# Kernel tuning notes

Measured on AMD Instinct MI355X. Metric: run time of the kernel, lower is better.

Reference implementation:

```python
import jax, jax.numpy as jnp
import numpy as np

N, E, IN_C, DIM, OUT_C, G = 40000, 640000, 128, 128, 16, 256
BN_EPS = 1e-5

def setup_inputs() -> dict:
    key = jax.random.key(0)
    ks = jax.random.split(key, 24)
    x = jax.random.normal(ks[0], (N, IN_C), dtype=jnp.float32)
    edge_index = jax.random.randint(ks[1], (2, E), 0, N, dtype=jnp.int32)
    batch = jnp.sort(jax.random.randint(ks[2], (N,), 0, G, dtype=jnp.int32))
    s = 1.0 / np.sqrt(DIM)
    # layer 1 (in_channels -> dim)
    W1_0 = jax.random.uniform(ks[3], (IN_C, DIM), jnp.float32, -s, s)
    b1_0 = jnp.zeros((DIM,), jnp.float32)
    g_0 = jnp.ones((DIM,), jnp.float32)
    bt_0 = jnp.zeros((DIM,), jnp.float32)
    W2_0 = jax.random.uniform(ks[4], (DIM, DIM), jnp.float32, -s, s)
    b2_0 = jnp.zeros((DIM,), jnp.float32)
    # layers 2-5 stacked (dim -> dim)
    W1s = jax.random.uniform(ks[5], (4, DIM, DIM), jnp.float32, -s, s)
    b1s = jnp.zeros((4, DIM), jnp.float32)
    gs = jnp.ones((4, DIM), jnp.float32)
    bts = jnp.zeros((4, DIM), jnp.float32)
    W2s = jax.random.uniform(ks[6], (4, DIM, DIM), jnp.float32, -s, s)
    b2s = jnp.zeros((4, DIM), jnp.float32)
    lin1_W = jax.random.uniform(ks[7], (DIM, DIM), jnp.float32, -s, s)
    lin1_b = jnp.zeros((DIM,), jnp.float32)
    lin2_W = jax.random.uniform(ks[8], (DIM, OUT_C), jnp.float32, -s, s)
    lin2_b = jnp.zeros((OUT_C,), jnp.float32)
    return dict(x=x, edge_index=edge_index, batch=batch, num_graphs=G,
                W1_0=W1_0, b1_0=b1_0, g_0=g_0, bt_0=bt_0, W2_0=W2_0, b2_0=b2_0,
                W1s=W1s, b1s=b1s, gs=gs, bts=bts, W2s=W2s, b2s=b2s,
                lin1_W=lin1_W, lin1_b=lin1_b, lin2_W=lin2_W, lin2_b=lin2_b)

def _gin_layer(x, src, dst, W1, b1, g, bt, W2, b2):
    # GIN aggregation: (1 + eps) * x_i + sum_{j in N(i)} x_j, eps = 0
    agg = jax.ops.segment_sum(x[src], dst, num_segments=x.shape[0])
    h = (x + agg) @ W1 + b1
    # BatchNorm1d over nodes (training-mode batch stats, biased variance)
    mu = h.mean(axis=0)
    var = h.var(axis=0)
    h = (h - mu) * jax.lax.rsqrt(var + BN_EPS) * g + bt
    h = jax.nn.relu(h)
    return jax.nn.relu(h @ W2 + b2)

def reference(x, edge_index, batch, num_graphs,
              W1_0, b1_0, g_0, bt_0, W2_0, b2_0,
              W1s, b1s, gs, bts, W2s, b2s,
              lin1_W, lin1_b, lin2_W, lin2_b):
    src, dst = edge_index[0], edge_index[1]
    h = _gin_layer(x, src, dst, W1_0, b1_0, g_0, bt_0, W2_0, b2_0)
    for i in range(4):
        h = _gin_layer(h, src, dst, W1s[i], b1s[i], gs[i], bts[i], W2s[i], b2s[i])
    x1 = h  # dropout p=0.2 in eval mode = identity
    pooled = jax.ops.segment_sum(x1, batch, num_segments=num_graphs)  # [G, DIM]
    out = jax.nn.relu(pooled @ lin1_W + lin1_b)
    out = out @ lin2_W + lin2_b
    return (jax.nn.log_softmax(out, axis=-1), x1)
```

## Files before the change

### kernel.cpp

```cpp
#include <hip/hip_runtime.h>

namespace {

constexpr int N    = 40000;
constexpr int E    = 640000;
constexpr int DIM  = 128;
constexpr int NG   = 256;
constexpr int OUTC = 16;
constexpr float BN_EPS = 1e-5f;

typedef __attribute__((ext_vector_type(8))) short bf16x8;
typedef __attribute__((ext_vector_type(4))) float f32x4;
typedef __attribute__((ext_vector_type(2))) float f32x2;

__device__ __forceinline__ void atomAddF(float* p, float v) {
  unsafeAtomicAdd(p, v);
}

__device__ __forceinline__ unsigned b16r(float f) {
  unsigned u = __float_as_uint(f);
  return (u + 0x7fffu + ((u >> 16) & 1u)) >> 16;
}
__device__ __forceinline__ unsigned pack2(float a, float b) {
  return b16r(a) | (b16r(b) << 16);
}

__device__ __forceinline__ unsigned pk4_fp8(float4 v) {
  unsigned u = __builtin_amdgcn_cvt_pk_fp8_f32(v.x, v.y, 0, false);
  u = __builtin_amdgcn_cvt_pk_fp8_f32(v.z, v.w, u, true);
  return u;
}
__device__ __forceinline__ void addfp8x4(float* a, unsigned u) {
  f32x2 lo = __builtin_amdgcn_cvt_pk_f32_fp8(u, false);
  f32x2 hi = __builtin_amdgcn_cvt_pk_f32_fp8(u, true);
  a[0] += lo[0]; a[1] += lo[1]; a[2] += hi[0]; a[3] += hi[1];
}
__device__ __forceinline__ void add16(float* a, const uint4 v) {
  addfp8x4(a, v.x); addfp8x4(a + 4, v.y); addfp8x4(a + 8, v.z); addfp8x4(a + 12, v.w);
}

__device__ __forceinline__ bf16x8 bnrelu8(bf16x8 a, const float* sc, const float* sh) {
  union { bf16x8 v; unsigned u[4]; } in, out;
  in.v = a;
#pragma unroll
  for (int p = 0; p < 4; ++p) {
    float lo = __uint_as_float(in.u[p] << 16);
    float hi = __uint_as_float(in.u[p] & 0xffff0000u);
    lo = fmaxf(fmaf(lo, sc[2 * p], sh[2 * p]), 0.f);
    hi = fmaxf(fmaf(hi, sc[2 * p + 1], sh[2 * p + 1]), 0.f);
    out.u[p] = pack2(lo, hi);
  }
  return out.v;
}

constexpr int CVT_B   = (N * DIM / 4) / 256;
constexpr int HIST_B  = E / 256;
constexpr int TRANS_B = 10 * DIM / 4;

__global__ __launch_bounds__(256) void prep_kernel(const float* __restrict__ x,
                                                   unsigned char* __restrict__ xf8,
                                                   const int* __restrict__ dst,
                                                   int* __restrict__ deg,
                                                   const float* __restrict__ W1_0,
                                                   const float* __restrict__ W2_0,
                                                   const float* __restrict__ W1s,
                                                   const float* __restrict__ W2s,
                                                   ushort* __restrict__ Wt) {
  const int b = blockIdx.x;
  if (b < CVT_B) {
    const int i = b * 256 + threadIdx.x;
    float4 v = ((const float4*)x)[i];
    ((unsigned*)xf8)[i] = pk4_fp8(v);
  } else if (b < CVT_B + HIST_B) {
    const int e = (b - CVT_B) * 256 + threadIdx.x;
    atomicAdd(&deg[dst[e]], 1);
  } else {
    const int ob   = (b - CVT_B - HIST_B) * 4 + (threadIdx.x >> 6);
    const int lane = threadIdx.x & 63;
    const int m = ob >> 7;
    const int c = ob & 127;
    const int l = m >> 1;
    const float* W;
    if (l == 0) W = (m & 1) ? W2_0 : W1_0;
    else        W = ((m & 1) ? W2s : W1s) + (size_t)(l - 1) * DIM * DIM;
    const int k = lane * 2;
    float f0 = W[(size_t)k * DIM + c];
    float f1 = W[(size_t)(k + 1) * DIM + c];
    ((unsigned*)Wt)[((size_t)m * DIM + c) * 64 + lane] = pack2(f0, f1);
  }
}


__global__ __launch_bounds__(256) void alloc_kernel(const int* __restrict__ deg,
                                                    int* __restrict__ counter,
                                                    int* __restrict__ start,
                                                    int* __restrict__ cursor) {
  const int i    = blockIdx.x * blockDim.x + threadIdx.x;
  const int lane = threadIdx.x & 63;
  int d = (i < N) ? deg[i] : 0;
  int incl = d;
#pragma unroll
  for (int o = 1; o < 64; o <<= 1) {
    int v = __shfl_up(incl, o, 64);
    if (lane >= o) incl += v;
  }
  int base = 0;
  if (lane == 63) base = atomicAdd(counter, incl);
  base = __shfl(base, 63, 64);
  int s0 = base + incl - d;
  if (i < N) { start[i] = s0; cursor[i] = s0; }
}

__global__ void fill_kernel(const int* __restrict__ src, const int* __restrict__ dst,
                            int* __restrict__ cursor, int* __restrict__ col) {
  int e = blockIdx.x * blockDim.x + threadIdx.x;
  if (e < E) {
    int p = atomicAdd(&cursor[dst[e]], 1);
    col[p] = src[e];
  }
}


__global__ __launch_bounds__(512) void gin1_fused(const unsigned char* __restrict__ xf8,
                                                  const int* __restrict__ start,
                                                  const int* __restrict__ deg,
                                                  const int* __restrict__ col,
                                                  const ushort* __restrict__ Wt1,
                                                  const float* __restrict__ b1,
                                                  ushort* __restrict__ h,
                                                  float* __restrict__ stats8) {
  __shared__ uint4 tile4[64 * 16];
  const int tid   = threadIdx.x;
  const int node0 = blockIdx.x * 64;

  {
    const int r = tid >> 3;
    const int l = tid & 7;
    const int node = node0 + r;
    const uint4* __restrict__ x16 = (const uint4*)xf8;
    float a[16];
#pragma unroll
    for (int i = 0; i < 16; ++i) a[i] = 0.f;
    add16(a, x16[(size_t)node * 8 + l]);
    const int b = start[node], n = deg[node];
    int k = 0;
    for (; k + 4 <= n; k += 4) {
      int j0 = col[b + k], j1 = col[b + k + 1], j2 = col[b + k + 2], j3 = col[b + k + 3];
      uint4 v0 = x16[(size_t)j0 * 8 + l];
      uint4 v1 = x16[(size_t)j1 * 8 + l];
      uint4 v2 = x16[(size_t)j2 * 8 + l];
      uint4 v3 = x16[(size_t)j3 * 8 + l];
      add16(a, v0); add16(a, v1); add16(a, v2); add16(a, v3);
    }
    for (; k < n; ++k) add16(a, x16[(size_t)col[b + k] * 8 + l]);
    uint4 o0 = {pack2(a[0], a[1]), pack2(a[2], a[3]), pack2(a[4], a[5]), pack2(a[6], a[7])};
    uint4 o1 = {pack2(a[8], a[9]), pack2(a[10], a[11]), pack2(a[12], a[13]), pack2(a[14], a[15])};
    const int sw = (r << 1) & 15;
    tile4[r * 16 + ((2 * l) ^ sw)]     = o0;
    tile4[r * 16 + ((2 * l + 1) ^ sw)] = o1;
  }
  __syncthreads();

  const int w    = tid >> 6;
  const int lane = tid & 63;
  const int rh   = __builtin_amdgcn_readfirstlane(w >> 2);
  const int c0   = __builtin_amdgcn_readfirstlane((w & 3) * 32);
  const int lr   = lane & 15;
  const int lg   = lane >> 4;

  const ushort* __restrict__ brow = Wt1 + (size_t)(c0 + lr) * DIM + lg * 8;
  const bf16x8* __restrict__ tb   = (const bf16x8*)tile4;

  f32x4 acc00 = {0, 0, 0, 0}, acc01 = {0, 0, 0, 0}, acc10 = {0, 0, 0, 0}, acc11 = {0, 0, 0, 0};
  const int r0 = rh * 32 + lr, r1 = rh * 32 + 16 + lr;
  const int sw0 = (r0 << 1) & 15, sw1 = (r1 << 1) & 15;
#pragma unroll
  for (int ks = 0; ks < 4; ++ks) {
    bf16x8 a0 = tb[r0 * 16 + ((lg + ks * 4) ^ sw0)];
    bf16x8 a1 = tb[r1 * 16 + ((lg + ks * 4) ^ sw1)];
    bf16x8 b0 = *(const bf16x8*)(brow + ks * 32);
    bf16x8 b1v = *(const bf16x8*)(brow + 16 * DIM + ks * 32);
    acc00 = __builtin_amdgcn_mfma_f32_16x16x32_bf16(a0, b0, acc00, 0, 0, 0);
    acc01 = __builtin_amdgcn_mfma_f32_16x16x32_bf16(a0, b1v, acc01, 0, 0, 0);
    acc10 = __builtin_amdgcn_mfma_f32_16x16x32_bf16(a1, b0, acc10, 0, 0, 0);
    acc11 = __builtin_amdgcn_mfma_f32_16x16x32_bf16(a1, b1v, acc11, 0, 0, 0);
  }

  const float bia0 = b1[c0 + lr];
  const float bia1 = b1[c0 + 16 + lr];
  float s[2] = {0, 0}, q[2] = {0, 0};
  f32x4 accs[2][2] = {{acc00, acc01}, {acc10, acc11}};
#pragma unroll
  for (int rf = 0; rf < 2; ++rf) {
#pragma unroll
    for (int cf = 0; cf < 2; ++cf) {
      const int colidx = c0 + cf * 16 + lr;
      const float bb = cf ? bia1 : bia0;
#pragma unroll
      for (int rg = 0; rg < 4; ++rg) {
        float v = accs[rf][cf][rg] + bb;
        const int row = node0 + rh * 32 + rf * 16 + lg * 4 + rg;
        h[(size_t)row * DIM + colidx] = (ushort)b16r(v);
        s[cf] += v; q[cf] = fmaf(v, v, q[cf]);
      }
    }
  }
#pragma unroll
  for (int cf = 0; cf < 2; ++cf) {
    float ss = s[cf], qq = q[cf];
    ss += __shfl_xor(ss, 16); ss += __shfl_xor(ss, 32);
    qq += __shfl_xor(qq, 16); qq += __shfl_xor(qq, 32);
    if (lg == 0) {
      float* st = stats8 + (blockIdx.x & 7) * 2 * DIM;
      atomAddF(&st[c0 + cf * 16 + lr], ss);
      atomAddF(&st[DIM + c0 + cf * 16 + lr], qq);
    }
  }
}


template <int F32OUT>
__global__ __launch_bounds__(256) void gin2_fused(const ushort* __restrict__ h,
                                                  const float* __restrict__ stats8,
                                                  const float* __restrict__ gamma,
                                                  const float* __restrict__ beta,
                                                  const ushort* __restrict__ Wt2,
                                                  const float* __restrict__ b2,
                                                  unsigned char* __restrict__ xf8,
                                                  float* __restrict__ outf) {
  __shared__ float lsc[DIM], lsh[DIM];
  const int tid = threadIdx.x;
  if (tid < DIM) {
    float s = 0.f, q = 0.f;
#pragma unroll
    for (int p = 0; p < 8; ++p) {
      s += stats8[p * 2 * DIM + tid];
      q += stats8[p * 2 * DIM + DIM + tid];
    }
    const float inv_n = 1.0f / N;
    float mu  = s * inv_n;
    float var = q * inv_n - mu * mu;
    float sc  = gamma[tid] * rsqrtf(var + BN_EPS);
    lsc[tid] = sc;
    lsh[tid] = beta[tid] - mu * sc;
  }
  __syncthreads();

  const int lane = tid & 63;
  const int c0   = __builtin_amdgcn_readfirstlane((tid >> 6) * 32);
  const int lr   = lane & 15;
  const int lg   = lane >> 4;
  const int row0 = blockIdx.x * 32;

  const ushort* __restrict__ arow = h + (size_t)(row0 + lr) * DIM + lg * 8;
  const ushort* __restrict__ brow = Wt2 + (size_t)(c0 + lr) * DIM + lg * 8;

  f32x4 acc00 = {0, 0, 0, 0}, acc01 = {0, 0, 0, 0}, acc10 = {0, 0, 0, 0}, acc11 = {0, 0, 0, 0};

#pragma unroll
  for (int ks = 0; ks < 4; ++ks) {
    const int ch0 = lg * 8 + ks * 32;
    float sc[8], sh[8];
    *(float4*)(sc)     = *(const float4*)&lsc[ch0];
    *(float4*)(sc + 4) = *(const float4*)&lsc[ch0 + 4];
    *(float4*)(sh)     = *(const float4*)&lsh[ch0];
    *(float4*)(sh + 4) = *(const float4*)&lsh[ch0 + 4];
    bf16x8 a0 = bnrelu8(*(const bf16x8*)(arow + ks * 32), sc, sh);
    bf16x8 a1 = bnrelu8(*(const bf16x8*)(arow + 16 * DIM + ks * 32), sc, sh);
    bf16x8 b0 = *(const bf16x8*)(brow + ks * 32);
    bf16x8 b1 = *(const bf16x8*)(brow + 16 * DIM + ks * 32);
    acc00 = __builtin_amdgcn_mfma_f32_16x16x32_bf16(a0, b0, acc00, 0, 0, 0);
    acc01 = __builtin_amdgcn_mfma_f32_16x16x32_bf16(a0, b1, acc01, 0, 0, 0);
    acc10 = __builtin_amdgcn_mfma_f32_16x16x32_bf16(a1, b0, acc10, 0, 0, 0);
    acc11 = __builtin_amdgcn_mfma_f32_16x16x32_bf16(a1, b1, acc11, 0, 0, 0);
  }

  const float bia0 = b2[c0 + lr];
  const float bia1 = b2[c0 + 16 + lr];
  f32x4 accs[2][2] = {{acc00, acc01}, {acc10, acc11}};
#pragma unroll
  for (int rf = 0; rf < 2; ++rf) {
#pragma unroll
    for (int cf = 0; cf < 2; ++cf) {
      const int colidx = c0 + cf * 16 + lr;
      const float bb = cf ? bia1 : bia0;
#pragma unroll
      for (int rg = 0; rg < 4; ++rg) {
        float v = fmaxf(accs[rf][cf][rg] + bb, 0.f);
        const int row = row0 + rf * 16 + lg * 4 + rg;
        if (F32OUT) {
          outf[(size_t)row * DIM + colidx] = v;
        } else {
          float vp = __shfl_xor(v, 1);
          if (!(lr & 1)) {
            unsigned pk = __builtin_amdgcn_cvt_pk_fp8_f32(v, vp, 0, false);
            *(ushort*)(xf8 + (size_t)row * DIM + colidx) = (ushort)pk;
          }
        }
      }
    }
  }
}


__global__ __launch_bounds__(256) void pool_kernel(const float* __restrict__ x1,
                                                   const int* __restrict__ batch,
                                                   float* __restrict__ pooled) {
  const int grp  = (blockIdx.x * blockDim.x + threadIdx.x) >> 5;
  const int lane = threadIdx.x & 31;
  const int node0 = grp * 64;
  if (node0 >= N) return;
  const int end = (node0 + 64 < N) ? (node0 + 64) : N;
  float4 acc = {0, 0, 0, 0};
  int cur = batch[node0];
  for (int n = node0; n < end; ++n) {
    int b = batch[n];
    if (b != cur) {
      atomAddF(&pooled[(size_t)cur * DIM + lane * 4 + 0], acc.x);
      atomAddF(&pooled[(size_t)cur * DIM + lane * 4 + 1], acc.y);
      atomAddF(&pooled[(size_t)cur * DIM + lane * 4 + 2], acc.z);
      atomAddF(&pooled[(size_t)cur * DIM + lane * 4 + 3], acc.w);
      acc = {0, 0, 0, 0};
      cur = b;
    }
    float4 v = ((const float4*)x1)[(size_t)n * 32 + lane];
    acc.x += v.x; acc.y += v.y; acc.z += v.z; acc.w += v.w;
  }
  atomAddF(&pooled[(size_t)cur * DIM + lane * 4 + 0], acc.x);
  atomAddF(&pooled[(size_t)cur * DIM + lane * 4 + 1], acc.y);
  atomAddF(&pooled[(size_t)cur * DIM + lane * 4 + 2], acc.z);
  atomAddF(&pooled[(size_t)cur * DIM + lane * 4 + 3], acc.w);
}


__global__ __launch_bounds__(128) void mlp_kernel(const float* __restrict__ pooled,
                                                  const float* __restrict__ W1,
                                                  const float* __restrict__ b1,
                                                  const float* __restrict__ W2,
                                                  const float* __restrict__ b2,
                                                  float* __restrict__ out) {
  const int gidx = blockIdx.x;
  const int t    = threadIdx.x;
  __shared__ float p[DIM], a1[DIM];
  p[t] = pooled[(size_t)gidx * DIM + t];
  __syncthreads();
  float acc = b1[t];
  for (int k = 0; k < DIM; ++k) acc = fmaf(p[k], W1[(size_t)k * DIM + t], acc);
  a1[t] = fmaxf(acc, 0.f);
  __syncthreads();
  if (t < OUTC) {
    float o = b2[t];
    for (int k = 0; k < DIM; ++k) o = fmaf(a1[k], W2[(size_t)k * OUTC + t], o);
    float m = o;
    for (int s = 8; s >= 1; s >>= 1) m = fmaxf(m, __shfl_xor(m, s, 16));
    float e = __expf(o - m);
    float se = e;
    for (int s = 8; s >= 1; s >>= 1) se += __shfl_xor(se, s, 16);
    out[(size_t)gidx * OUTC + t] = o - m - __logf(se);
  }
}

}

extern "C" void kernel_launch(void* const* d_in, const int* in_sizes, int n_in,
                              void* d_out, int out_size, void* d_ws, size_t ws_size,
                              hipStream_t stream) {
  const float* x     = (const float*)d_in[0];
  const int*   ei    = (const int*)d_in[1];
  const int*   batch = (const int*)d_in[2];
  const float* W1_0  = (const float*)d_in[4];
  const float* b1_0  = (const float*)d_in[5];
  const float* g_0   = (const float*)d_in[6];
  const float* bt_0  = (const float*)d_in[7];
  const float* W2_0  = (const float*)d_in[8];
  const float* b2_0  = (const float*)d_in[9];
  const float* W1s   = (const float*)d_in[10];
  const float* b1s   = (const float*)d_in[11];
  const float* gs    = (const float*)d_in[12];
  const float* bts   = (const float*)d_in[13];
  const float* W2s   = (const float*)d_in[14];
  const float* b2s   = (const float*)d_in[15];
  const float* lin1W = (const float*)d_in[16];
  const float* lin1b = (const float*)d_in[17];
  const float* lin2W = (const float*)d_in[18];
  const float* lin2b = (const float*)d_in[19];

  float* out_ls = (float*)d_out;
  float* x1_out = (float*)d_out + NG * OUTC;

  char* w = (char*)d_ws;
  auto alloc = [&](size_t bytes) -> void* {
    void* p = (void*)w;
    w += (bytes + 255) & ~(size_t)255;
    return p;
  };
  int*    deg      = (int*)alloc((size_t)(N + 64) * 4);
  int*    counter  = deg + N;
  float*  statsAll = (float*)alloc((size_t)(5 * 8 * 2 * DIM + NG * DIM) * 4);
  float*  pooled   = statsAll + 5 * 8 * 2 * DIM;
  const size_t zero_bytes = (size_t)(N + 64) * 4 + (size_t)(5 * 8 * 2 * DIM + NG * DIM) * 4;

  int*    start  = (int*)alloc((size_t)N * 4);
  int*    cursor = (int*)alloc((size_t)N * 4);
  int*    col    = (int*)alloc((size_t)E * 4);
  unsigned char* xf8 = (unsigned char*)alloc((size_t)N * DIM);
  ushort* act    = (ushort*)alloc((size_t)N * DIM * 2);
  ushort* Wt     = (ushort*)alloc((size_t)10 * DIM * DIM * 2);

  const int* src = ei;
  const int* dst = ei + E;

  hipMemsetAsync(deg, 0, zero_bytes, stream);

  prep_kernel<<<CVT_B + HIST_B + TRANS_B, 256, 0, stream>>>(x, xf8, dst, deg,
                                                            W1_0, W2_0, W1s, W2s, Wt);
  alloc_kernel<<<(N + 255) / 256, 256, 0, stream>>>(deg, counter, start, cursor);
  fill_kernel<<<E / 256, 256, 0, stream>>>(src, dst, cursor, col);

  for (int l = 0; l < 5; ++l) {
    const float* b1 = (l == 0) ? b1_0 : b1s + (size_t)(l - 1) * DIM;
    const float* gg = (l == 0) ? g_0  : gs  + (size_t)(l - 1) * DIM;
    const float* bb = (l == 0) ? bt_0 : bts + (size_t)(l - 1) * DIM;
    const float* b2 = (l == 0) ? b2_0 : b2s + (size_t)(l - 1) * DIM;
    const ushort* Wt1 = Wt + (size_t)(2 * l) * DIM * DIM;
    const ushort* Wt2 = Wt + (size_t)(2 * l + 1) * DIM * DIM;
    float* stats8 = statsAll + (size_t)l * 8 * 2 * DIM;

    gin1_fused<<<N / 64, 512, 0, stream>>>(xf8, start, deg, col, Wt1, b1, act, stats8);
    if (l == 4)
      gin2_fused<1><<<N / 32, 256, 0, stream>>>(act, stats8, gg, bb, Wt2, b2, nullptr, x1_out);
    else
      gin2_fused<0><<<N / 32, 256, 0, stream>>>(act, stats8, gg, bb, Wt2, b2, xf8, nullptr);
  }

  {
    int groups = (N + 63) / 64;
    int blocks = (groups * 32 + 255) / 256;
    pool_kernel<<<blocks, 256, 0, stream>>>(x1_out, batch, pooled);
  }
  mlp_kernel<<<NG, 128, 0, stream>>>(pooled, lin1W, lin1b, lin2W, lin2b, out_ls);
}
```

Baseline: 316.5 us.

## Split fp8 features into column slabs and gather in two passes

The fp8 node feature buffer is stored as two column slabs of 64 channels each, so each gather pass reads a 64-byte row half. The aggregation in gin1_fused now uses 4 threads per node looping over the two slabs, with 256 threads per block. The MFMA stage is retiled so each wave covers 32 rows by 64 columns, and the LDS swizzle is changed to match. The intent is to shrink the working set of each gather pass for better cache hit rates, at the cost of reading the neighbor index list twice, having fewer threads in flight, and more accumulators per wave.

```diff
diff --git a/kernel.cpp b/kernel.cpp
--- a/kernel.cpp
+++ b/kernel.cpp
@@ -8,6 +8,7 @@
 constexpr int NG   = 256;
 constexpr int OUTC = 16;
 constexpr float BN_EPS = 1e-5f;
+constexpr size_t SLAB = (size_t)N * 64;
 
 typedef __attribute__((ext_vector_type(8))) short bf16x8;
 typedef __attribute__((ext_vector_type(4))) float f32x4;
@@ -37,6 +38,10 @@
 }
 __device__ __forceinline__ void add16(float* a, const uint4 v) {
   addfp8x4(a, v.x); addfp8x4(a + 4, v.y); addfp8x4(a + 8, v.z); addfp8x4(a + 12, v.w);
+}
+
+__device__ __forceinline__ int rot4(int r) {
+  return ((r << 1) | ((r >> 3) & 1)) & 15;
 }
 
 __device__ __forceinline__ bf16x8 bnrelu8(bf16x8 a, const float* sc, const float* sh) {
@@ -70,7 +75,10 @@
   if (b < CVT_B) {
     const int i = b * 256 + threadIdx.x;
     float4 v = ((const float4*)x)[i];
-    ((unsigned*)xf8)[i] = pk4_fp8(v);
+    const int row = i >> 5;
+    const int c0  = (i & 31) * 4;
+    ((unsigned*)xf8)[(size_t)(c0 >> 6) * (N * 16) + (size_t)row * 16 + ((c0 & 63) >> 2)] =
+        pk4_fp8(v);
   } else if (b < CVT_B + HIST_B) {
     const int e = (b - CVT_B) * 256 + threadIdx.x;
     atomicAdd(&deg[dst[e]], 1);
@@ -121,7 +129,7 @@
 }
 
 
-__global__ __launch_bounds__(512) void gin1_fused(const unsigned char* __restrict__ xf8,
+__global__ __launch_bounds__(256) void gin1_fused(const unsigned char* __restrict__ xf8,
                                                   const int* __restrict__ start,
                                                   const int* __restrict__ deg,
                                                   const int* __restrict__ col,
@@ -134,71 +142,78 @@
   const int node0 = blockIdx.x * 64;
 
   {
-    const int r = tid >> 3;
-    const int l = tid & 7;
+    const int r = tid >> 2;
+    const int l = tid & 3;
     const int node = node0 + r;
-    const uint4* __restrict__ x16 = (const uint4*)xf8;
-    float a[16];
-#pragma unroll
-    for (int i = 0; i < 16; ++i) a[i] = 0.f;
-    add16(a, x16[(size_t)node * 8 + l]);
     const int b = start[node], n = deg[node];
-    int k = 0;
-    for (; k + 4 <= n; k += 4) {
-      int j0 = col[b + k], j1 = col[b + k + 1], j2 = col[b + k + 2], j3 = col[b + k + 3];
-      uint4 v0 = x16[(size_t)j0 * 8 + l];
-      uint4 v1 = x16[(size_t)j1 * 8 + l];
-      uint4 v2 = x16[(size_t)j2 * 8 + l];
-      uint4 v3 = x16[(size_t)j3 * 8 + l];
-      add16(a, v0); add16(a, v1); add16(a, v2); add16(a, v3);
-    }
-    for (; k < n; ++k) add16(a, x16[(size_t)col[b + k] * 8 + l]);
-    uint4 o0 = {pack2(a[0], a[1]), pack2(a[2], a[3]), pack2(a[4], a[5]), pack2(a[6], a[7])};
-    uint4 o1 = {pack2(a[8], a[9]), pack2(a[10], a[11]), pack2(a[12], a[13]), pack2(a[14], a[15])};
-    const int sw = (r << 1) & 15;
-    tile4[r * 16 + ((2 * l) ^ sw)]     = o0;
-    tile4[r * 16 + ((2 * l + 1) ^ sw)] = o1;
+    const int sw = rot4(r);
+#pragma unroll 1
+    for (int s = 0; s < 2; ++s) {
+      const uint4* __restrict__ x16 = (const uint4*)(xf8 + (size_t)s * SLAB);
+      float a[16];
+#pragma unroll
+      for (int i = 0; i < 16; ++i) a[i] = 0.f;
+      add16(a, x16[(size_t)node * 4 + l]);
+      int k = 0;
+      for (; k + 4 <= n; k += 4) {
+        int j0 = col[b + k], j1 = col[b + k + 1], j2 = col[b + k + 2], j3 = col[b + k + 3];
+        uint4 v0 = x16[(size_t)j0 * 4 + l];
+        uint4 v1 = x16[(size_t)j1 * 4 + l];
+        uint4 v2 = x16[(size_t)j2 * 4 + l];
+        uint4 v3 = x16[(size_t)j3 * 4 + l];
+        add16(a, v0); add16(a, v1); add16(a, v2); add16(a, v3);
+      }
+      for (; k < n; ++k) add16(a, x16[(size_t)col[b + k] * 4 + l]);
+      uint4 o0 = {pack2(a[0], a[1]), pack2(a[2], a[3]), pack2(a[4], a[5]), pack2(a[6], a[7])};
+      uint4 o1 = {pack2(a[8], a[9]), pack2(a[10], a[11]), pack2(a[12], a[13]), pack2(a[14], a[15])};
+      const int cb = s * 8 + 2 * l;
+      tile4[r * 16 + (cb ^ sw)]       = o0;
+      tile4[r * 16 + ((cb + 1) ^ sw)] = o1;
+    }
   }
   __syncthreads();
 
   const int w    = tid >> 6;
   const int lane = tid & 63;
-  const int rh   = __builtin_amdgcn_readfirstlane(w >> 2);
-  const int c0   = __builtin_amdgcn_readfirstlane((w & 3) * 32);
+  const int rh   = __builtin_amdgcn_readfirstlane(w >> 1);
+  const int c0   = __builtin_amdgcn_readfirstlane((w & 1) * 64);
   const int lr   = lane & 15;
   const int lg   = lane >> 4;
 
+  const bf16x8* __restrict__ tb = (const bf16x8*)tile4;
+  const int r0 = rh * 32 + lr, r1 = r0 + 16;
+  const int sw0 = rot4(r0 & 15);
+
   const ushort* __restrict__ brow = Wt1 + (size_t)(c0 + lr) * DIM + lg * 8;
-  const bf16x8* __restrict__ tb   = (const bf16x8*)tile4;
-
-  f32x4 acc00 = {0, 0, 0, 0}, acc01 = {0, 0, 0, 0}, acc10 = {0, 0, 0, 0}, acc11 = {0, 0, 0, 0};
-  const int r0 = rh * 32 + lr, r1 = rh * 32 + 16 + lr;
-  const int sw0 = (r0 << 1) & 15, sw1 = (r1 << 1) & 15;
+
+  f32x4 acc[2][4];
+#pragma unroll
+  for (int i = 0; i < 2; ++i)
+#pragma unroll
+    for (int j = 0; j < 4; ++j) acc[i][j] = {0, 0, 0, 0};
+
 #pragma unroll
   for (int ks = 0; ks < 4; ++ks) {
     bf16x8 a0 = tb[r0 * 16 + ((lg + ks * 4) ^ sw0)];
-    bf16x8 a1 = tb[r1 * 16 + ((lg + ks * 4) ^ sw1)];
-    bf16x8 b0 = *(const bf16x8*)(brow + ks * 32);
-    bf16x8 b1v = *(const bf16x8*)(brow + 16 * DIM + ks * 32);
-    acc00 = __builtin_amdgcn_mfma_f32_16x16x32_bf16(a0, b0, acc00, 0, 0, 0);
-    acc01 = __builtin_amdgcn_mfma_f32_16x16x32_bf16(a0, b1v, acc01, 0, 0, 0);
-    acc10 = __builtin_amdgcn_mfma_f32_16x16x32_bf16(a1, b0, acc10, 0, 0, 0);
-    acc11 = __builtin_amdgcn_mfma_f32_16x16x32_bf16(a1, b1v, acc11, 0, 0, 0);
-  }
-
-  const float bia0 = b1[c0 + lr];
-  const float bia1 = b1[c0 + 16 + lr];
-  float s[2] = {0, 0}, q[2] = {0, 0};
-  f32x4 accs[2][2] = {{acc00, acc01}, {acc10, acc11}};
+    bf16x8 a1 = tb[r1 * 16 + ((lg + ks * 4) ^ sw0)];
+#pragma unroll
+    for (int cf = 0; cf < 4; ++cf) {
+      bf16x8 bf = *(const bf16x8*)(brow + (size_t)cf * 16 * DIM + ks * 32);
+      acc[0][cf] = __builtin_amdgcn_mfma_f32_16x16x32_bf16(a0, bf, acc[0][cf], 0, 0, 0);
+      acc[1][cf] = __builtin_amdgcn_mfma_f32_16x16x32_bf16(a1, bf, acc[1][cf], 0, 0, 0);
+    }
+  }
+
+  float s[4] = {0, 0, 0, 0}, q[4] = {0, 0, 0, 0};
 #pragma unroll
   for (int rf = 0; rf < 2; ++rf) {
 #pragma unroll
-    for (int cf = 0; cf < 2; ++cf) {
+    for (int cf = 0; cf < 4; ++cf) {
       const int colidx = c0 + cf * 16 + lr;
-      const float bb = cf ? bia1 : bia0;
+      const float bb = b1[colidx];
 #pragma unroll
       for (int rg = 0; rg < 4; ++rg) {
-        float v = accs[rf][cf][rg] + bb;
+        float v = acc[rf][cf][rg] + bb;
         const int row = node0 + rh * 32 + rf * 16 + lg * 4 + rg;
         h[(size_t)row * DIM + colidx] = (ushort)b16r(v);
         s[cf] += v; q[cf] = fmaf(v, v, q[cf]);
@@ -206,7 +221,7 @@
     }
   }
 #pragma unroll
-  for (int cf = 0; cf < 2; ++cf) {
+  for (int cf = 0; cf < 4; ++cf) {
     float ss = s[cf], qq = q[cf];
     ss += __shfl_xor(ss, 16); ss += __shfl_xor(ss, 32);
     qq += __shfl_xor(qq, 16); qq += __shfl_xor(qq, 32);
@@ -294,7 +309,9 @@
           float vp = __shfl_xor(v, 1);
           if (!(lr & 1)) {
             unsigned pk = __builtin_amdgcn_cvt_pk_fp8_f32(v, vp, 0, false);
-            *(ushort*)(xf8 + (size_t)row * DIM + colidx) = (ushort)pk;
+            unsigned char* dp = xf8 + (size_t)(colidx >> 6) * SLAB +
+                                (size_t)row * 64 + (colidx & 63);
+            *(ushort*)dp = (ushort)pk;
           }
         }
       }
@@ -403,7 +420,7 @@
   int*    start  = (int*)alloc((size_t)N * 4);
   int*    cursor = (int*)alloc((size_t)N * 4);
   int*    col    = (int*)alloc((size_t)E * 4);
-  unsigned char* xf8 = (unsigned char*)alloc((size_t)N * DIM);
+  unsigned char* xf8 = (unsigned char*)alloc(2 * SLAB);
   ushort* act    = (ushort*)alloc((size_t)N * DIM * 2);
   ushort* Wt     = (ushort*)alloc((size_t)10 * DIM * DIM * 2);
 
@@ -426,7 +443,7 @@
     const ushort* Wt2 = Wt + (size_t)(2 * l + 1) * DIM * DIM;
     float* stats8 = statsAll + (size_t)l * 8 * 2 * DIM;
 
-    gin1_fused<<<N / 64, 512, 0, stream>>>(xf8, start, deg, col, Wt1, b1, act, stats8);
+    gin1_fused<<<N / 64, 256, 0, stream>>>(xf8, start, deg, col, Wt1, b1, act, stats8);
     if (l == 4)
       gin2_fused<1><<<N / 32, 256, 0, stream>>>(act, stats8, gg, bb, Wt2, b2, nullptr, x1_out);
     else
```

New measurement: 314.8 us. Within noise of the previous version (-0.5%).
